# Performance work log

Measured on AMD Instinct MI355X. Metric: run time of the kernel, lower is better.

Reference implementation:

```python
import jax, jax.numpy as jnp
import numpy as np

B, S = 64, 512
VOCAB, D, H, NH = 50000, 256, 256, 4
MAX_DUR = 12.0
SCALE_RATE = 1.0


def setup_inputs() -> dict:
    key = jax.random.key(0)
    ks = jax.random.split(key, 12)
    s = 1.0 / np.sqrt(H)
    inp = {
        "src": jax.random.randint(ks[0], (B, S), 0, VOCAB),
        "input_len": jax.random.randint(ks[1], (B,), 1, S + 1),
        "fix_src": jax.random.uniform(ks[2], (B, S), jnp.float32) * MAX_DUR,
        "emb_table": jax.random.normal(ks[3], (VOCAB, D), jnp.float32) * 0.02,
        "Wi": jax.random.uniform(ks[4], (H, D), jnp.float32, -s, s),
        "bi": jax.random.uniform(ks[5], (H,), jnp.float32, -s, s),
        "Wh": jax.random.uniform(ks[6], (H, NH * H), jnp.float32, -s, s),
        "bh": jax.random.uniform(ks[7], (H,), jnp.float32, -s, s),
        "fc1_W": jax.random.uniform(ks[8], (D, NH * H), jnp.float32, -s, s),
        "fc1_b": jax.random.uniform(ks[9], (D,), jnp.float32, -s, s),
        "fc2_W": jax.random.uniform(ks[10], (2, D), jnp.float32, -s, s),
        "fc2_b": jax.random.uniform(ks[11], (2,), jnp.float32, -s, s),
    }
    return inp


def _forward(src, input_len, fix_src, emb_table, Wi, bi, Wh, bh, fc1_W, fc1_b, fc2_W, fc2_b):
    emb = emb_table[src]                      # [B, S, D]
    offsets = jnp.arange(NH, dtype=emb.dtype) * (MAX_DUR / NH)  # [NH]
    h0 = jnp.zeros((NH, B, H), emb.dtype)

    def step(h, xd):
        x, d = xd                             # x [B,D], d [B]
        hcat = jnp.swapaxes(h, 0, 1).reshape(B, NH * H)
        cand = jnp.tanh(x @ Wi.T + bi + hcat @ Wh.T + bh)        # [B,H]
        g = jax.nn.sigmoid(d[:, None] * SCALE_RATE - offsets)    # [B,NH]
        gt = g.T[:, :, None]                                     # [NH,B,1]
        h_new = gt * cand[None, :, :] + (1.0 - gt) * h           # [NH,B,H]
        out = jnp.swapaxes(h_new, 0, 1).reshape(B, NH * H)
        return h_new, out

    xs = (jnp.swapaxes(emb, 0, 1), fix_src.T)  # [S,B,D], [S,B]
    _, outs = jax.lax.scan(step, h0, xs)       # [S, B, NH*H]
    outs = jnp.swapaxes(outs, 0, 1)            # [B, S, NH*H]
    sel = outs[jnp.arange(B), input_len - 1]   # gather at last valid step, [B, NH*H]
    hid = jnp.tanh(sel @ fc1_W.T + fc1_b)      # [B, D]
    return hid @ fc2_W.T + fc2_b               # [B, 2]


def reference(src, input_len, fix_src, emb_table, Wi, bi, Wh, bh, fc1_W, fc1_b, fc2_W, fc2_b):
    return _forward(src, input_len, fix_src, emb_table, Wi, bi, Wh, bh, fc1_W, fc1_b, fc2_W, fc2_b)
```

## Files before the change

kernel.cpp:

```cpp
#include <hip/hip_runtime.h>
#include <stdint.h>

constexpr int BB = 64;
constexpr int SS = 512;
constexpr int DD = 256;
constexpr int HH = 256;
constexpr int NHH = 4;
constexpr int KK = 1024;

constexpr int TT = 512;

typedef _Float16 f16;
typedef _Float16 f16x2 __attribute__((ext_vector_type(2)));
typedef _Float16 half8 __attribute__((ext_vector_type(8)));
typedef float f32x4 __attribute__((ext_vector_type(4)));

__device__ inline float dot2p(uint32_t a, uint32_t b, float c) {
  f16x2 av = __builtin_bit_cast(f16x2, a);
  f16x2 bv = __builtin_bit_cast(f16x2, b);
#if defined(__has_builtin)
#if __has_builtin(__builtin_amdgcn_fdot2)
  return __builtin_amdgcn_fdot2(av, bv, c, false);
#else
  return c + (float)av.x * (float)bv.x + (float)av.y * (float)bv.y;
#endif
#else
  return c + (float)av.x * (float)bv.x + (float)av.y * (float)bv.y;
#endif
}

__device__ inline float dot8(uint4 w, uint4 a, float c) {
  c = dot2p(w.x, a.x, c);
  c = dot2p(w.y, a.y, c);
  c = dot2p(w.z, a.z, c);
  c = dot2p(w.w, a.w, c);
  return c;
}

__device__ inline uint32_t pack2(float a, float b) {
  f16x2 v;
  v.x = (f16)a;
  v.y = (f16)b;
  return __builtin_bit_cast(uint32_t, v);
}

__device__ inline float fast_tanh(float x) {
  x = fminf(fmaxf(x, -15.f), 15.f);
  float e = __expf(2.f * x);
  return 1.f - 2.f / (e + 1.f);
}

__global__ void k_pack_wq(const float* __restrict__ Wh, uint4* __restrict__ Wq) {
  int gid = blockIdx.x * blockDim.x + threadIdx.x;
  int p = gid >> 13;
  int m = (gid >> 9) & 15;
  int t = gid & 511;
  int out = t & 255, ch2 = t >> 8;
  int n = out >> 6, o_loc = out & 63;
  const float* s = Wh + (64 * p + o_loc) * KK + 256 * n + 128 * ch2 + 8 * m;
  uint4 w;
  w.x = pack2(s[0], s[1]);
  w.y = pack2(s[2], s[3]);
  w.z = pack2(s[4], s[5]);
  w.w = pack2(s[6], s[7]);
  Wq[gid] = w;
}

__global__ void k_transpose8(const float* __restrict__ src, float* __restrict__ dst,
                             int C, int total) {
  int gid = blockIdx.x * blockDim.x + threadIdx.x;
  if (gid >= total) return;
  int r = gid & 255, c = gid >> 8;
  dst[gid] = src[r * C + c];
}

__global__ void k_cvt_f16(const float* __restrict__ src, f16* __restrict__ dst,
                          int total) {
  int gid = blockIdx.x * blockDim.x + threadIdx.x;
  if (gid >= total) return;
  dst[gid] = (f16)src[gid];
}

__global__ __launch_bounds__(256) void k_u_mfma(
    const int* __restrict__ src, const float* __restrict__ emb,
    const f16* __restrict__ wif, const float* __restrict__ bi,
    const float* __restrict__ bh, const int* __restrict__ input_len,
    f16* __restrict__ U) {
  __shared__ __align__(16) char xls[32768];
  const int row0 = blockIdx.x * 64;
  const int b = row0 >> 9;
  if ((row0 & 511) >= input_len[b]) return;
  const int t = threadIdx.x;
  const int w = t >> 6, l = t & 63;

  for (int rr = 0; rr < 16; ++rr) {
    int r = w * 16 + rr;
    int srcid = src[row0 + r];
    const float4 x = *(const float4*)(emb + (size_t)srcid * DD + l * 4);
    uint2 dw;
    dw.x = pack2(x.x, x.y);
    dw.y = pack2(x.z, x.w);
    int byte = (r * 512 + l * 8) ^ ((r & 7) << 4);
    *(uint2*)(xls + byte) = dw;
  }
  __syncthreads();

  const int lm = l & 15, lk = l >> 4;
  const int arow = w * 16 + lm;
  const int xs = (arow & 7) << 4;

  for (int ct = 0; ct < 16; ++ct) {
    const int o = ct * 16 + lm;
    f32x4 acc = {0.f, 0.f, 0.f, 0.f};
    const f16* bp = wif + (size_t)o * 256 + lk * 8;
#pragma unroll
    for (int kt = 0; kt < 8; ++kt) {
      int ab = (arow * 512 + kt * 64 + lk * 16) ^ xs;
      half8 af = *(const half8*)(xls + ab);
      half8 bf = *(const half8*)(bp + kt * 32);
      acc = __builtin_amdgcn_mfma_f32_16x16x32_f16(af, bf, acc, 0, 0, 0);
    }
    float bias = bi[o] + bh[o];
#pragma unroll
    for (int reg = 0; reg < 4; ++reg) {
      int grow = row0 + w * 16 + lk * 4 + reg;
      U[(size_t)grow * HH + o] = (f16)(acc[reg] + bias);
    }
  }
}

__global__ void __attribute__((amdgpu_flat_work_group_size(512, 512),
                               amdgpu_waves_per_eu(2, 2)))
k_recurrence(
    const uint4* __restrict__ Wq, const f16* __restrict__ U,
    const float* __restrict__ fix_src, const int* __restrict__ input_len,
    const float* __restrict__ fc1T, const float* __restrict__ fc1_b,
    const float* __restrict__ fc2_W, const float* __restrict__ fc2_b,
    float* __restrict__ out, uint32_t* __restrict__ Cex,
    float* __restrict__ FPg, int* __restrict__ Flg) {
  __shared__ __align__(16) char arena[61440];
  f16* cbuf = (f16*)arena;
  uint4* cvec = (uint4*)arena;
  float* partials = (float*)(arena + 512);
  float* hbuf = (float*)(arena + 2560);

  const int idx = blockIdx.x;
  const int b = idx & 63;
  const int p = idx >> 6;
  const int t = threadIdx.x;
  const int out_i = t & 255, ch2 = t >> 8;
  const int n = out_i >> 6, o_loc = out_i & 63;

  uint4 w[16];
  {
    const uint4* wp = Wq + (p * 16) * TT + t;
#pragma unroll
    for (int m = 0; m < 16; ++m) {
      const uint4* a = wp + m * TT;
      asm volatile("global_load_dwordx4 %0, %1, off"
                   : "=v"(w[m]) : "v"(a) : "memory");
    }
    asm volatile("s_waitcnt vmcnt(0)" ::: "memory");
  }

  float v0 = 0.f, v1 = 0.f, v2 = 0.f, v3 = 0.f;
  float h = 0.f;

  const int len = input_len[b];
  const f16* Ub = U + (size_t)b * SS * HH;
  const float* fsb = fix_src + b * SS;

  if (t < 64) {
    float c0 = fast_tanh((float)Ub[64 * p + t]);
    f16 chv = (f16)c0;
    cbuf[64 * p + t] = chv;
    uint32_t dwp =
        ((uint32_t)__builtin_bit_cast(unsigned short, chv) << 16) | 1u;
    __hip_atomic_store(&Cex[b * 256 + p * 64 + t], dwp, __ATOMIC_RELAXED,
                       __HIP_MEMORY_SCOPE_AGENT);
  }

#pragma unroll 1
  for (int s = 0; s < len; ++s) {
#pragma unroll
    for (int m = 0; m < 16; ++m)
      asm volatile("" : "+v"(w[m].x), "+v"(w[m].y), "+v"(w[m].z), "+v"(w[m].w));

    const int par = s & 1;
    const uint32_t tag = (uint32_t)((s + 1) & 0xffff);
    const float dval = fsb[s];
    float g = 0.f, gq1 = 0.f, gq2 = 0.f, gq3 = 0.f, ufn = 0.f;

    if (t < 64) {
      int sn = (s + 1 < len) ? (s + 1) : s;
      ufn = (float)Ub[(size_t)sn * HH + 64 * p + t];
      g   = 1.f / (1.f + __expf(0.f - dval));
      gq1 = 1.f / (1.f + __expf(3.f - dval));
      gq2 = 1.f / (1.f + __expf(6.f - dval));
      gq3 = 1.f / (1.f + __expf(9.f - dval));
    } else if (t < 256) {
      g = 1.f / (1.f + __expf((float)(3 * n) - dval));
      int wv = t >> 6;
      int lane = t & 63;
      int q = (p + wv) & 3;
      uint32_t* addr = &Cex[((par * 64 + b) * 4 + q) * 64 + lane];
      uint32_t dw;
      do {
        dw = __hip_atomic_load(addr, __ATOMIC_RELAXED,
                               __HIP_MEMORY_SCOPE_AGENT);
      } while ((dw & 0xffffu) != tag);
      cbuf[64 * q + lane] =
          __builtin_bit_cast(f16, (unsigned short)(dw >> 16));
    }
    __syncthreads();

    float acc = 0.f;
    const uint4* ap = cvec + ch2 * 16;
#pragma unroll
    for (int m = 0; m < 16; ++m) acc = dot8(w[m], ap[m], acc);
    partials[t] = acc;

    if (t < 256) {
      float cown = (float)cbuf[64 * p + o_loc];
      h = g * cown + (1.f - g) * h;
    }
    __syncthreads();

    if (t < 64) {
      float w0 = partials[t]       + partials[256 + t];
      float w1 = partials[64 + t]  + partials[320 + t];
      float w2 = partials[128 + t] + partials[384 + t];
      float w3 = partials[192 + t] + partials[448 + t];
      v0 = g   * w0 + (1.f - g)   * v0;
      v1 = gq1 * w1 + (1.f - gq1) * v1;
      v2 = gq2 * w2 + (1.f - gq2) * v2;
      v3 = gq3 * w3 + (1.f - gq3) * v3;
      float c = fast_tanh(ufn + (v0 + v1 + v2 + v3));
      f16 chv = (f16)c;
      uint32_t dwp =
          ((uint32_t)__builtin_bit_cast(unsigned short, chv) << 16) |
          (uint32_t)((s + 2) & 0xffff);
      __hip_atomic_store(
          &Cex[(((s + 1) & 1) * 64 + b) * 256 + p * 64 + t], dwp,
          __ATOMIC_RELAXED, __HIP_MEMORY_SCOPE_AGENT);
      cbuf[64 * p + t] = chv;
    }
  }

  if (t < 256) hbuf[out_i] = h;
  __syncthreads();
  {
    float acc = 0.f;
#pragma unroll 4
    for (int r = 0; r < 128; ++r) {
      int k_loc = ch2 * 128 + r;
      int n2 = k_loc >> 6, il = k_loc & 63;
      int kg = n2 * 256 + 64 * p + il;
      acc += hbuf[k_loc] * fc1T[(size_t)kg * 256 + out_i];
    }
    partials[t] = acc;
  }
  __syncthreads();
  if (t < 256) FPg[(b * 4 + p) * 256 + out_i] =
      partials[out_i] + partials[256 + out_i];
  __syncthreads();
  if (t == 0)
    __hip_atomic_store(&Flg[b * 4 + p], 0x5A5A5A5A, __ATOMIC_RELEASE,
                       __HIP_MEMORY_SCOPE_AGENT);
  if (p != 0) return;
  if (t < 4 && t > 0) {
    while (__hip_atomic_load(&Flg[b * 4 + t], __ATOMIC_ACQUIRE,
                             __HIP_MEMORY_SCOPE_AGENT) != 0x5A5A5A5A) {
    }
  }
  __syncthreads();
  if (t < 256) {
    float pre = fc1_b[t];
#pragma unroll
    for (int q = 0; q < 4; ++q)
      pre += __hip_atomic_load(&FPg[(b * 4 + q) * 256 + t], __ATOMIC_RELAXED,
                               __HIP_MEMORY_SCOPE_AGENT);
    hbuf[t] = fast_tanh(pre);
  }
  __syncthreads();
  if (t < 64) {
    float p0 = 0.f, p1 = 0.f;
    for (int oi = t; oi < 256; oi += 64) {
      float hh = hbuf[oi];
      p0 += hh * fc2_W[oi];
      p1 += hh * fc2_W[256 + oi];
    }
#pragma unroll
    for (int off = 32; off; off >>= 1) {
      p0 += __shfl_down(p0, off);
      p1 += __shfl_down(p1, off);
    }
    if (t == 0) {
      out[b * 2 + 0] = p0 + fc2_b[0];
      out[b * 2 + 1] = p1 + fc2_b[1];
    }
  }
}

extern "C" void kernel_launch(void* const* d_in, const int* in_sizes, int n_in,
                              void* d_out, int out_size, void* d_ws, size_t ws_size,
                              hipStream_t stream) {
  const int* src = (const int*)d_in[0];
  const int* input_len = (const int*)d_in[1];
  const float* fix_src = (const float*)d_in[2];
  const float* emb = (const float*)d_in[3];
  const float* Wi = (const float*)d_in[4];
  const float* bi = (const float*)d_in[5];
  const float* Wh = (const float*)d_in[6];
  const float* bh = (const float*)d_in[7];
  const float* fc1_W = (const float*)d_in[8];
  const float* fc1_b = (const float*)d_in[9];
  const float* fc2_W = (const float*)d_in[10];
  const float* fc2_b = (const float*)d_in[11];
  float* out = (float*)d_out;

  char* ws = (char*)d_ws;
  uint4* Wq = (uint4*)(ws);
  f16* wif = (f16*)(ws + (512ull << 10));
  float* fc1T = (float*)(ws + (768ull << 10));
  f16* U = (f16*)(ws + (1792ull << 10));
  uint32_t* Cex = (uint32_t*)(ws + (18176ull << 10));
  float* FPg = (float*)(ws + (18304ull << 10));
  int* Flg = (int*)(ws + (18560ull << 10));
  const size_t needed = (18561ull << 10);
  if (ws_size < needed) return;

  k_pack_wq<<<128, 256, 0, stream>>>(Wh, Wq);
  k_cvt_f16<<<(65536 + 255) / 256, 256, 0, stream>>>(Wi, wif, 65536);
  k_transpose8<<<(262144 + 255) / 256, 256, 0, stream>>>(fc1_W, fc1T, 1024, 262144);
  k_u_mfma<<<BB * SS / 64, 256, 0, stream>>>(src, emb, wif, bi, bh,
                                             input_len, U);
  k_recurrence<<<BB * 4, TT, 0, stream>>>(Wq, U, fix_src, input_len, fc1T,
                                          fc1_b, fc2_W, fc2_b, out, Cex, FPg,
                                          Flg);
}
```

Measured before the change: 719.9 us.

## Process two batch rows per recurrence workgroup, halving the grid to 128 blocks

```diff
diff --git a/kernel.cpp b/kernel.cpp
--- a/kernel.cpp
+++ b/kernel.cpp
@@ -139,14 +139,18 @@
     float* __restrict__ out, uint32_t* __restrict__ Cex,
     float* __restrict__ FPg, int* __restrict__ Flg) {
   __shared__ __align__(16) char arena[61440];
-  f16* cbuf = (f16*)arena;
-  uint4* cvec = (uint4*)arena;
-  float* partials = (float*)(arena + 512);
-  float* hbuf = (float*)(arena + 2560);
+  f16* cbufA = (f16*)arena;
+  f16* cbufB = (f16*)(arena + 512);
+  uint4* cvecA = (uint4*)arena;
+  uint4* cvecB = (uint4*)(arena + 512);
+  float* partials = (float*)(arena + 1024);
+  float* hbufA = (float*)(arena + 3072);
+  float* hbufB = (float*)(arena + 4096);
 
   const int idx = blockIdx.x;
-  const int b = idx & 63;
-  const int p = idx >> 6;
+  const int g = idx & 31;
+  const int p = idx >> 5;
+  const int bA = g, bB = g + 32;
   const int t = threadIdx.x;
   const int out_i = t & 255, ch2 = t >> 8;
   const int n = out_i >> 6, o_loc = out_i & 63;
@@ -163,91 +167,169 @@
     asm volatile("s_waitcnt vmcnt(0)" ::: "memory");
   }
 
-  float v0 = 0.f, v1 = 0.f, v2 = 0.f, v3 = 0.f;
-  float h = 0.f;
-
-  const int len = input_len[b];
-  const f16* Ub = U + (size_t)b * SS * HH;
-  const float* fsb = fix_src + b * SS;
+  float vA0 = 0.f, vA1 = 0.f, vA2 = 0.f, vA3 = 0.f;
+  float vB0 = 0.f, vB1 = 0.f, vB2 = 0.f, vB3 = 0.f;
+  float hA = 0.f, hB = 0.f;
+
+  const int lenA = input_len[bA];
+  const int lenB = input_len[bB];
+  const int smax = (lenA > lenB) ? lenA : lenB;
+  const f16* UbA = U + (size_t)bA * SS * HH;
+  const f16* UbB = U + (size_t)bB * SS * HH;
+  const float* fsA = fix_src + bA * SS;
+  const float* fsB = fix_src + bB * SS;
 
   if (t < 64) {
-    float c0 = fast_tanh((float)Ub[64 * p + t]);
+    float c0 = fast_tanh((float)UbA[64 * p + t]);
     f16 chv = (f16)c0;
-    cbuf[64 * p + t] = chv;
+    cbufA[64 * p + t] = chv;
     uint32_t dwp =
         ((uint32_t)__builtin_bit_cast(unsigned short, chv) << 16) | 1u;
-    __hip_atomic_store(&Cex[b * 256 + p * 64 + t], dwp, __ATOMIC_RELAXED,
+    __hip_atomic_store(&Cex[bA * 256 + p * 64 + t], dwp, __ATOMIC_RELAXED,
                        __HIP_MEMORY_SCOPE_AGENT);
+    float c0b = fast_tanh((float)UbB[64 * p + t]);
+    f16 chvb = (f16)c0b;
+    cbufB[64 * p + t] = chvb;
+    uint32_t dwpb =
+        ((uint32_t)__builtin_bit_cast(unsigned short, chvb) << 16) | 1u;
+    __hip_atomic_store(&Cex[bB * 256 + p * 64 + t], dwpb, __ATOMIC_RELAXED,
+                       __HIP_MEMORY_SCOPE_AGENT);
   }
 
 #pragma unroll 1
-  for (int s = 0; s < len; ++s) {
+  for (int s = 0; s < smax; ++s) {
 #pragma unroll
     for (int m = 0; m < 16; ++m)
       asm volatile("" : "+v"(w[m].x), "+v"(w[m].y), "+v"(w[m].z), "+v"(w[m].w));
 
     const int par = s & 1;
     const uint32_t tag = (uint32_t)((s + 1) & 0xffff);
-    const float dval = fsb[s];
-    float g = 0.f, gq1 = 0.f, gq2 = 0.f, gq3 = 0.f, ufn = 0.f;
-
-    if (t < 64) {
-      int sn = (s + 1 < len) ? (s + 1) : s;
-      ufn = (float)Ub[(size_t)sn * HH + 64 * p + t];
-      g   = 1.f / (1.f + __expf(0.f - dval));
-      gq1 = 1.f / (1.f + __expf(3.f - dval));
-      gq2 = 1.f / (1.f + __expf(6.f - dval));
-      gq3 = 1.f / (1.f + __expf(9.f - dval));
-    } else if (t < 256) {
-      g = 1.f / (1.f + __expf((float)(3 * n) - dval));
-      int wv = t >> 6;
-      int lane = t & 63;
-      int q = (p + wv) & 3;
-      uint32_t* addr = &Cex[((par * 64 + b) * 4 + q) * 64 + lane];
-      uint32_t dw;
-      do {
-        dw = __hip_atomic_load(addr, __ATOMIC_RELAXED,
-                               __HIP_MEMORY_SCOPE_AGENT);
-      } while ((dw & 0xffffu) != tag);
-      cbuf[64 * q + lane] =
-          __builtin_bit_cast(f16, (unsigned short)(dw >> 16));
-    }
-    __syncthreads();
-
-    float acc = 0.f;
-    const uint4* ap = cvec + ch2 * 16;
-#pragma unroll
-    for (int m = 0; m < 16; ++m) acc = dot8(w[m], ap[m], acc);
-    partials[t] = acc;
-
-    if (t < 256) {
-      float cown = (float)cbuf[64 * p + o_loc];
-      h = g * cown + (1.f - g) * h;
-    }
-    __syncthreads();
-
-    if (t < 64) {
-      float w0 = partials[t]       + partials[256 + t];
-      float w1 = partials[64 + t]  + partials[320 + t];
-      float w2 = partials[128 + t] + partials[384 + t];
-      float w3 = partials[192 + t] + partials[448 + t];
-      v0 = g   * w0 + (1.f - g)   * v0;
-      v1 = gq1 * w1 + (1.f - gq1) * v1;
-      v2 = gq2 * w2 + (1.f - gq2) * v2;
-      v3 = gq3 * w3 + (1.f - gq3) * v3;
-      float c = fast_tanh(ufn + (v0 + v1 + v2 + v3));
-      f16 chv = (f16)c;
-      uint32_t dwp =
-          ((uint32_t)__builtin_bit_cast(unsigned short, chv) << 16) |
-          (uint32_t)((s + 2) & 0xffff);
-      __hip_atomic_store(
-          &Cex[(((s + 1) & 1) * 64 + b) * 256 + p * 64 + t], dwp,
-          __ATOMIC_RELAXED, __HIP_MEMORY_SCOPE_AGENT);
-      cbuf[64 * p + t] = chv;
-    }
-  }
-
-  if (t < 256) hbuf[out_i] = h;
+
+    {
+      const bool act = s < lenA;
+      float g0 = 0.f, gq1 = 0.f, gq2 = 0.f, gq3 = 0.f, ufn = 0.f;
+      if (act) {
+        const float dval = fsA[s];
+        if (t < 64) {
+          int sn = (s + 1 < lenA) ? (s + 1) : s;
+          ufn = (float)UbA[(size_t)sn * HH + 64 * p + t];
+          g0  = 1.f / (1.f + __expf(0.f - dval));
+          gq1 = 1.f / (1.f + __expf(3.f - dval));
+          gq2 = 1.f / (1.f + __expf(6.f - dval));
+          gq3 = 1.f / (1.f + __expf(9.f - dval));
+        } else if (t < 256) {
+          g0 = 1.f / (1.f + __expf((float)(3 * n) - dval));
+          int wv = t >> 6, lane = t & 63;
+          int q = (p + wv) & 3;
+          const int off = ((par * 64 + bA) * 4 + q) * 64 + lane;
+          uint32_t dw;
+          do {
+            dw = __hip_atomic_load(&Cex[off], __ATOMIC_RELAXED,
+                                   __HIP_MEMORY_SCOPE_AGENT);
+          } while ((dw & 0xffffu) != tag);
+          cbufA[64 * q + lane] =
+              __builtin_bit_cast(f16, (unsigned short)(dw >> 16));
+        }
+      }
+      __syncthreads();
+      if (act) {
+        float acc = 0.f;
+        const uint4* ap = cvecA + ch2 * 16;
+#pragma unroll
+        for (int m = 0; m < 16; ++m) acc = dot8(w[m], ap[m], acc);
+        partials[t] = acc;
+        if (t < 256) {
+          float cown = (float)cbufA[64 * p + o_loc];
+          hA = g0 * cown + (1.f - g0) * hA;
+        }
+      }
+      __syncthreads();
+      if (act && t < 64) {
+        float w0 = partials[t]       + partials[256 + t];
+        float w1 = partials[64 + t]  + partials[320 + t];
+        float w2 = partials[128 + t] + partials[384 + t];
+        float w3 = partials[192 + t] + partials[448 + t];
+        vA0 = g0  * w0 + (1.f - g0)  * vA0;
+        vA1 = gq1 * w1 + (1.f - gq1) * vA1;
+        vA2 = gq2 * w2 + (1.f - gq2) * vA2;
+        vA3 = gq3 * w3 + (1.f - gq3) * vA3;
+        float c = fast_tanh(ufn + (vA0 + vA1 + vA2 + vA3));
+        f16 chv = (f16)c;
+        uint32_t dwp =
+            ((uint32_t)__builtin_bit_cast(unsigned short, chv) << 16) |
+            (uint32_t)((s + 2) & 0xffff);
+        const int po = (((s + 1) & 1) * 64 + bA) * 256 + p * 64 + t;
+        __hip_atomic_store(&Cex[po], dwp, __ATOMIC_RELAXED,
+                           __HIP_MEMORY_SCOPE_AGENT);
+        cbufA[64 * p + t] = chv;
+      }
+    }
+
+    {
+      const bool act = s < lenB;
+      float g0 = 0.f, gq1 = 0.f, gq2 = 0.f, gq3 = 0.f, ufn = 0.f;
+      if (act) {
+        const float dval = fsB[s];
+        if (t < 64) {
+          int sn = (s + 1 < lenB) ? (s + 1) : s;
+          ufn = (float)UbB[(size_t)sn * HH + 64 * p + t];
+          g0  = 1.f / (1.f + __expf(0.f - dval));
+          gq1 = 1.f / (1.f + __expf(3.f - dval));
+          gq2 = 1.f / (1.f + __expf(6.f - dval));
+          gq3 = 1.f / (1.f + __expf(9.f - dval));
+        } else if (t < 256) {
+          g0 = 1.f / (1.f + __expf((float)(3 * n) - dval));
+          int wv = t >> 6, lane = t & 63;
+          int q = (p + wv) & 3;
+          const int off = ((par * 64 + bB) * 4 + q) * 64 + lane;
+          uint32_t dw;
+          do {
+            dw = __hip_atomic_load(&Cex[off], __ATOMIC_RELAXED,
+                                   __HIP_MEMORY_SCOPE_AGENT);
+          } while ((dw & 0xffffu) != tag);
+          cbufB[64 * q + lane] =
+              __builtin_bit_cast(f16, (unsigned short)(dw >> 16));
+        }
+      }
+      __syncthreads();
+      if (act) {
+        float acc = 0.f;
+        const uint4* ap = cvecB + ch2 * 16;
+#pragma unroll
+        for (int m = 0; m < 16; ++m) acc = dot8(w[m], ap[m], acc);
+        partials[t] = acc;
+        if (t < 256) {
+          float cown = (float)cbufB[64 * p + o_loc];
+          hB = g0 * cown + (1.f - g0) * hB;
+        }
+      }
+      __syncthreads();
+      if (act && t < 64) {
+        float w0 = partials[t]       + partials[256 + t];
+        float w1 = partials[64 + t]  + partials[320 + t];
+        float w2 = partials[128 + t] + partials[384 + t];
+        float w3 = partials[192 + t] + partials[448 + t];
+        vB0 = g0  * w0 + (1.f - g0)  * vB0;
+        vB1 = gq1 * w1 + (1.f - gq1) * vB1;
+        vB2 = gq2 * w2 + (1.f - gq2) * vB2;
+        vB3 = gq3 * w3 + (1.f - gq3) * vB3;
+        float c = fast_tanh(ufn + (vB0 + vB1 + vB2 + vB3));
+        f16 chv = (f16)c;
+        uint32_t dwp =
+            ((uint32_t)__builtin_bit_cast(unsigned short, chv) << 16) |
+            (uint32_t)((s + 2) & 0xffff);
+        const int po = (((s + 1) & 1) * 64 + bB) * 256 + p * 64 + t;
+        __hip_atomic_store(&Cex[po], dwp, __ATOMIC_RELAXED,
+                           __HIP_MEMORY_SCOPE_AGENT);
+        cbufB[64 * p + t] = chv;
+      }
+    }
+  }
+
+  if (t < 256) {
+    hbufA[out_i] = hA;
+    hbufB[out_i] = hB;
+  }
   __syncthreads();
   {
     float acc = 0.f;
@@ -256,37 +338,68 @@
       int k_loc = ch2 * 128 + r;
       int n2 = k_loc >> 6, il = k_loc & 63;
       int kg = n2 * 256 + 64 * p + il;
-      acc += hbuf[k_loc] * fc1T[(size_t)kg * 256 + out_i];
+      acc += hbufA[k_loc] * fc1T[(size_t)kg * 256 + out_i];
     }
     partials[t] = acc;
   }
   __syncthreads();
-  if (t < 256) FPg[(b * 4 + p) * 256 + out_i] =
+  if (t < 256) FPg[(bA * 4 + p) * 256 + out_i] =
       partials[out_i] + partials[256 + out_i];
   __syncthreads();
-  if (t == 0)
-    __hip_atomic_store(&Flg[b * 4 + p], 0x5A5A5A5A, __ATOMIC_RELEASE,
+  {
+    float acc = 0.f;
+#pragma unroll 4
+    for (int r = 0; r < 128; ++r) {
+      int k_loc = ch2 * 128 + r;
+      int n2 = k_loc >> 6, il = k_loc & 63;
+      int kg = n2 * 256 + 64 * p + il;
+      acc += hbufB[k_loc] * fc1T[(size_t)kg * 256 + out_i];
+    }
+    partials[t] = acc;
+  }
+  __syncthreads();
+  if (t < 256) FPg[(bB * 4 + p) * 256 + out_i] =
+      partials[out_i] + partials[256 + out_i];
+  __syncthreads();
+  if (t == 0) {
+    __hip_atomic_store(&Flg[bA * 4 + p], 0x5A5A5A5A, __ATOMIC_RELEASE,
                        __HIP_MEMORY_SCOPE_AGENT);
+    __hip_atomic_store(&Flg[bB * 4 + p], 0x5A5A5A5A, __ATOMIC_RELEASE,
+                       __HIP_MEMORY_SCOPE_AGENT);
+  }
   if (p != 0) return;
-  if (t < 4 && t > 0) {
-    while (__hip_atomic_load(&Flg[b * 4 + t], __ATOMIC_ACQUIRE,
+  if (t > 0 && t < 4) {
+    while (__hip_atomic_load(&Flg[bA * 4 + t], __ATOMIC_ACQUIRE,
                              __HIP_MEMORY_SCOPE_AGENT) != 0x5A5A5A5A) {
     }
+  } else if (t > 4 && t < 8) {
+    while (__hip_atomic_load(&Flg[bB * 4 + (t - 4)], __ATOMIC_ACQUIRE,
+                             __HIP_MEMORY_SCOPE_AGENT) != 0x5A5A5A5A) {
+    }
   }
   __syncthreads();
   if (t < 256) {
-    float pre = fc1_b[t];
-#pragma unroll
-    for (int q = 0; q < 4; ++q)
-      pre += __hip_atomic_load(&FPg[(b * 4 + q) * 256 + t], __ATOMIC_RELAXED,
-                               __HIP_MEMORY_SCOPE_AGENT);
-    hbuf[t] = fast_tanh(pre);
-  }
-  __syncthreads();
-  if (t < 64) {
+    float preA = fc1_b[t];
+    float preB = fc1_b[t];
+#pragma unroll
+    for (int q = 0; q < 4; ++q) {
+      preA += __hip_atomic_load(&FPg[(bA * 4 + q) * 256 + t], __ATOMIC_RELAXED,
+                                __HIP_MEMORY_SCOPE_AGENT);
+      preB += __hip_atomic_load(&FPg[(bB * 4 + q) * 256 + t], __ATOMIC_RELAXED,
+                                __HIP_MEMORY_SCOPE_AGENT);
+    }
+    hbufA[t] = fast_tanh(preA);
+    hbufB[t] = fast_tanh(preB);
+  }
+  __syncthreads();
+  if (t < 128) {
+    const int wv = t >> 6;
+    const int lane = t & 63;
+    const float* hb = wv ? hbufB : hbufA;
+    const int bo = wv ? bB : bA;
     float p0 = 0.f, p1 = 0.f;
-    for (int oi = t; oi < 256; oi += 64) {
-      float hh = hbuf[oi];
+    for (int oi = lane; oi < 256; oi += 64) {
+      float hh = hb[oi];
       p0 += hh * fc2_W[oi];
       p1 += hh * fc2_W[256 + oi];
     }
@@ -295,9 +408,9 @@
       p0 += __shfl_down(p0, off);
       p1 += __shfl_down(p1, off);
     }
-    if (t == 0) {
-      out[b * 2 + 0] = p0 + fc2_b[0];
-      out[b * 2 + 1] = p1 + fc2_b[1];
+    if (lane == 0) {
+      out[bo * 2 + 0] = p0 + fc2_b[0];
+      out[bo * 2 + 1] = p1 + fc2_b[1];
     }
   }
 }
@@ -335,7 +448,7 @@
   k_transpose8<<<(262144 + 255) / 256, 256, 0, stream>>>(fc1_W, fc1T, 1024, 262144);
   k_u_mfma<<<BB * SS / 64, 256, 0, stream>>>(src, emb, wif, bi, bh,
                                              input_len, U);
-  k_recurrence<<<BB * 4, TT, 0, stream>>>(Wq, U, fix_src, input_len, fc1T,
-                                          fc1_b, fc2_W, fc2_b, out, Cex, FPg,
-                                          Flg);
-}
+  k_recurrence<<<128, TT, 0, stream>>>(Wq, U, fix_src, input_len, fc1T,
+                                       fc1_b, fc2_W, fc2_b, out, Cex, FPg,
+                                       Flg);
+}
```

Measured after the change: 968.6 us. 34.5% more time.

## Repartition recurrent matvec so each wave handles a K-chunk across all four outputs

Applied to the files above, without the earlier changes.

```diff
diff --git a/kernel.cpp b/kernel.cpp
--- a/kernel.cpp
+++ b/kernel.cpp
@@ -55,9 +55,9 @@
   int p = gid >> 13;
   int m = (gid >> 9) & 15;
   int t = gid & 511;
-  int out = t & 255, ch2 = t >> 8;
-  int n = out >> 6, o_loc = out & 63;
-  const float* s = Wh + (64 * p + o_loc) * KK + 256 * n + 128 * ch2 + 8 * m;
+  int j = m >> 2, u = m & 3;
+  int wv = t >> 6, l = t & 63;
+  const float* s = Wh + (size_t)(64 * p + l) * KK + 256 * j + 32 * wv + 8 * u;
   uint4 w;
   w.x = pack2(s[0], s[1]);
   w.y = pack2(s[2], s[3]);
@@ -141,8 +141,9 @@
   __shared__ __align__(16) char arena[61440];
   f16* cbuf = (f16*)arena;
   uint4* cvec = (uint4*)arena;
+  float* part = (float*)(arena + 512);
   float* partials = (float*)(arena + 512);
-  float* hbuf = (float*)(arena + 2560);
+  float* hbuf = (float*)(arena + 8704);
 
   const int idx = blockIdx.x;
   const int b = idx & 63;
@@ -150,6 +151,7 @@
   const int t = threadIdx.x;
   const int out_i = t & 255, ch2 = t >> 8;
   const int n = out_i >> 6, o_loc = out_i & 63;
+  const int wv = t >> 6, l = t & 63;
 
   uint4 w[16];
   {
@@ -200,13 +202,13 @@
       gq3 = 1.f / (1.f + __expf(9.f - dval));
     } else if (t < 256) {
       g = 1.f / (1.f + __expf((float)(3 * n) - dval));
-      int wv = t >> 6;
+      int wvp = t >> 6;
       int lane = t & 63;
-      int q = (p + wv) & 3;
-      uint32_t* addr = &Cex[((par * 64 + b) * 4 + q) * 64 + lane];
+      int q = (p + wvp) & 3;
+      const int off = ((par * 64 + b) * 4 + q) * 64 + lane;
       uint32_t dw;
       do {
-        dw = __hip_atomic_load(addr, __ATOMIC_RELAXED,
+        dw = __hip_atomic_load(&Cex[off], __ATOMIC_RELAXED,
                                __HIP_MEMORY_SCOPE_AGENT);
       } while ((dw & 0xffffu) != tag);
       cbuf[64 * q + lane] =
@@ -214,11 +216,23 @@
     }
     __syncthreads();
 
-    float acc = 0.f;
-    const uint4* ap = cvec + ch2 * 16;
-#pragma unroll
-    for (int m = 0; m < 16; ++m) acc = dot8(w[m], ap[m], acc);
-    partials[t] = acc;
+    {
+      const uint4* ap = cvec + 4 * wv;
+      uint4 a0 = ap[0], a1 = ap[1], a2 = ap[2], a3 = ap[3];
+      float ac0 = 0.f, ac1 = 0.f, ac2 = 0.f, ac3 = 0.f;
+      ac0 = dot8(w[0], a0, ac0);  ac0 = dot8(w[1], a1, ac0);
+      ac0 = dot8(w[2], a2, ac0);  ac0 = dot8(w[3], a3, ac0);
+      ac1 = dot8(w[4], a0, ac1);  ac1 = dot8(w[5], a1, ac1);
+      ac1 = dot8(w[6], a2, ac1);  ac1 = dot8(w[7], a3, ac1);
+      ac2 = dot8(w[8], a0, ac2);  ac2 = dot8(w[9], a1, ac2);
+      ac2 = dot8(w[10], a2, ac2); ac2 = dot8(w[11], a3, ac2);
+      ac3 = dot8(w[12], a0, ac3); ac3 = dot8(w[13], a1, ac3);
+      ac3 = dot8(w[14], a2, ac3); ac3 = dot8(w[15], a3, ac3);
+      part[wv * 256 +   0 + l] = ac0;
+      part[wv * 256 +  64 + l] = ac1;
+      part[wv * 256 + 128 + l] = ac2;
+      part[wv * 256 + 192 + l] = ac3;
+    }
 
     if (t < 256) {
       float cown = (float)cbuf[64 * p + o_loc];
@@ -227,10 +241,15 @@
     __syncthreads();
 
     if (t < 64) {
-      float w0 = partials[t]       + partials[256 + t];
-      float w1 = partials[64 + t]  + partials[320 + t];
-      float w2 = partials[128 + t] + partials[384 + t];
-      float w3 = partials[192 + t] + partials[448 + t];
+      float w0 = 0.f, w1 = 0.f, w2 = 0.f, w3 = 0.f;
+#pragma unroll
+      for (int kc = 0; kc < 8; ++kc) {
+        const float* pr = part + kc * 256;
+        w0 += pr[t];
+        w1 += pr[64 + t];
+        w2 += pr[128 + t];
+        w3 += pr[192 + t];
+      }
       v0 = g   * w0 + (1.f - g)   * v0;
       v1 = gq1 * w1 + (1.f - gq1) * v1;
       v2 = gq2 * w2 + (1.f - gq2) * v2;
@@ -240,9 +259,9 @@
       uint32_t dwp =
           ((uint32_t)__builtin_bit_cast(unsigned short, chv) << 16) |
           (uint32_t)((s + 2) & 0xffff);
-      __hip_atomic_store(
-          &Cex[(((s + 1) & 1) * 64 + b) * 256 + p * 64 + t], dwp,
-          __ATOMIC_RELAXED, __HIP_MEMORY_SCOPE_AGENT);
+      const int po = (((s + 1) & 1) * 64 + b) * 256 + p * 64 + t;
+      __hip_atomic_store(&Cex[po], dwp, __ATOMIC_RELAXED,
+                         __HIP_MEMORY_SCOPE_AGENT);
       cbuf[64 * p + t] = chv;
     }
   }
```

Measured after the change: 721.6 us. About the same (+0.2%).
